# Performance work log

Hardware: AMD Instinct MI355X
Metric: run time of the kernel (lower is better)

The kernel has to match this reference:

```python
import jax, jax.numpy as jnp
import numpy as np
import math

B, L, LC = 2, 2048, 2048
D_MODEL, D_CROSS, D_HEAD = 1024, 1024, 64
N_HEADS = D_MODEL // D_HEAD
D6 = D_HEAD // 6  # freq bands per spatial axis (k-diffusion AxialRoPE, 3 axes)
EPS = 1e-6


def rope_freqs():
    n = N_HEADS * D6
    f = jnp.exp(jnp.linspace(math.log(math.pi), math.log(10.0 * math.pi), n + 1)[:-1])
    return f.reshape(D6, N_HEADS).T  # [nh, d6]


def rope_theta(pos):
    # pos: [b, l, 3] -> theta: [b, nh, l, 3*d6]
    f = rope_freqs()
    th = jnp.concatenate([pos[..., None, a:a + 1] * f for a in range(3)], axis=-1)  # [b,l,nh,3*d6]
    return jnp.moveaxis(th, -2, -3)


def apply_rotary(x, theta):
    d = theta.shape[-1]
    x1, x2, x3 = x[..., :d], x[..., d:2 * d], x[..., 2 * d:]
    c, s = jnp.cos(theta), jnp.sin(theta)
    return jnp.concatenate([x1 * c - x2 * s, x2 * c + x1 * s, x3], axis=-1)


def rms_norm(x, scale, eps=EPS):
    ms = jnp.mean(x * x, axis=-1, keepdims=True)
    return x * (scale * jax.lax.rsqrt(ms + eps))


def cosine_scale(q, k, scale, eps=EPS):
    s = jnp.sqrt(scale)[:, None, None]  # [nh,1,1]
    qn = q * (s * jax.lax.rsqrt(jnp.sum(q * q, axis=-1, keepdims=True) + eps))
    kn = k * (s * jax.lax.rsqrt(jnp.sum(k * k, axis=-1, keepdims=True) + eps))
    return qn, kn


def setup_inputs():
    key = jax.random.key(0)
    ks = jax.random.split(key, 8)
    return {
        "x": jax.random.normal(ks[0], (B, L, D_MODEL), jnp.float32),
        "pos": jax.random.uniform(ks[1], (B, L, 3), jnp.float32),
        "x_cross": jax.random.normal(ks[2], (B, LC, D_CROSS), jnp.float32),
        "pos_cross": jax.random.uniform(ks[3], (B, LC, 3), jnp.float32),
        "norm_scale": jnp.ones((D_MODEL,), jnp.float32),
        "norm_cross_scale": jnp.ones((D_CROSS,), jnp.float32),
        "q_w": jax.random.normal(ks[4], (D_MODEL, D_MODEL), jnp.float32) * 0.02,
        "kv_w": jax.random.normal(ks[5], (2 * D_MODEL, D_CROSS), jnp.float32) * 0.02,
        "head_scale": jnp.full((N_HEADS,), 10.0, jnp.float32),
        "out_w": jax.random.normal(ks[6], (D_MODEL, D_MODEL), jnp.float32) * 0.02,
    }


def reference(x, pos, x_cross, pos_cross, norm_scale, norm_cross_scale, q_w, kv_w, head_scale, out_w):
    skip = x
    xn = rms_norm(x, norm_scale)
    xc = rms_norm(x_cross, norm_cross_scale)
    q = xn @ q_w.T                       # [b,l,d]
    kv = xc @ kv_w.T                     # [b,lc,2d]
    b, l, _ = q.shape
    lc = kv.shape[1]
    q = q.reshape(b, l, N_HEADS, D_HEAD).transpose(0, 2, 1, 3)          # [b,nh,l,e]
    kv = kv.reshape(b, lc, 2, N_HEADS, D_HEAD)                          # (t nh e) factorization
    k = kv[:, :, 0].transpose(0, 2, 1, 3)
    v = kv[:, :, 1].transpose(0, 2, 1, 3)
    q, k = cosine_scale(q, k, head_scale)
    q = apply_rotary(q, rope_theta(pos))
    k = apply_rotary(k, rope_theta(pos_cross))
    attn = jax.nn.softmax(jnp.einsum('bhqe,bhke->bhqk', q, k), axis=-1)  # scale=1.0 (cosine-sim pre-scaled)
    o = jnp.einsum('bhqk,bhke->bhqe', attn, v)
    o = o.transpose(0, 2, 1, 3).reshape(b, l, D_MODEL)
    return o @ out_w.T + skip
```

## Files before the change

kernel.cpp:

```cpp
#include <hip/hip_runtime.h>

typedef __bf16 bf16_t;
typedef __bf16 bf16x4 __attribute__((ext_vector_type(4)));
typedef __bf16 bf16x8 __attribute__((ext_vector_type(8)));
typedef float f32x4 __attribute__((ext_vector_type(4)));
typedef short s16x4 __attribute__((ext_vector_type(4)));

#define B_DIM 2
#define L_DIM 2048
#define LC_DIM 2048
#define DM 1024
#define NH 16
#define DH 64
#define MB (1u << 20)
#define LOG2E 1.44269504088896f

__device__ __forceinline__ bool probe_is_f32(const unsigned* probe) {
  return probe[0] == 0x3F800000u;
}

__device__ __forceinline__ void async16(const bf16_t* g, bf16_t* l) {
  __builtin_amdgcn_global_load_lds((const __attribute__((address_space(1))) void*)g,
                                   (__attribute__((address_space(3))) void*)l, 16, 0, 0);
}

#if __has_builtin(__builtin_amdgcn_mfma_f32_16x16x16bf16_1k)
#define HAVE_K16 1
__device__ __forceinline__ f32x4 mfma16(bf16x4 a, bf16x4 b, f32x4 c) {
  union { bf16x4 h; s16x4 s; } ua, ub;
  ua.h = a; ub.h = b;
  return __builtin_amdgcn_mfma_f32_16x16x16bf16_1k(ua.s, ub.s, c, 0, 0, 0);
}
#else
#define HAVE_K16 0
#endif

__device__ __forceinline__ void conv_b(const void* src, bf16_t* dst, int i, bool f32) {
  bf16x4 w;
  if (f32) {
    f32x4 v = *(const f32x4*)((const float*)src + i);
    w[0] = (bf16_t)v[0]; w[1] = (bf16_t)v[1]; w[2] = (bf16_t)v[2]; w[3] = (bf16_t)v[3];
  } else {
    w = *(const bf16x4*)((const bf16_t*)src + i);
  }
  *(bf16x4*)(dst + i) = w;
}
__device__ __forceinline__ void conv_f(const void* src, float* dst, int i, int n, bool f32) {
  if (i >= n) return;
  f32x4 v;
  if (f32) {
    v = *(const f32x4*)((const float*)src + i);
  } else {
    bf16x4 w = *(const bf16x4*)((const bf16_t*)src + i);
    v[0] = (float)w[0]; v[1] = (float)w[1]; v[2] = (float)w[2]; v[3] = (float)w[3];
  }
  *(f32x4*)(dst + i) = v;
}

__global__ __launch_bounds__(256) void conv_all_k(
    const void* qw, const void* kvw, const void* ow, const void* pos,
    const void* posc, const void* ns, const void* ncs, const void* hs,
    bf16_t* cqw, bf16_t* ckvw, bf16_t* cow, float* fpos, float* fposc,
    float* fns, float* fncs, float* fhs, const unsigned* probe) {
  const bool f32 = probe_is_f32(probe);
  const int blk = blockIdx.x;
  const int e4 = threadIdx.x * 4;
  if (blk < 1024)       conv_b(qw,  cqw,  blk * 1024 + e4, f32);
  else if (blk < 3072)  conv_b(kvw, ckvw, (blk - 1024) * 1024 + e4, f32);
  else if (blk < 4096)  conv_b(ow,  cow,  (blk - 3072) * 1024 + e4, f32);
  else if (blk < 4108)  conv_f(pos,  fpos,  (blk - 4096) * 1024 + e4, 12288, f32);
  else if (blk < 4120)  conv_f(posc, fposc, (blk - 4108) * 1024 + e4, 12288, f32);
  else if (blk == 4120) conv_f(ns,  fns,  e4, 1024, f32);
  else if (blk == 4121) conv_f(ncs, fncs, e4, 1024, f32);
  else                  conv_f(hs,  fhs,  e4, 16, f32);
}

__global__ __launch_bounds__(256) void norm_both_k(const void* __restrict__ srcA,
                                                   const void* __restrict__ srcB,
                                                   const float* __restrict__ scA,
                                                   const float* __restrict__ scB,
                                                   bf16_t* __restrict__ outA,
                                                   bf16_t* __restrict__ outB,
                                                   const unsigned* __restrict__ probe) {
  const bool isB = blockIdx.x >= B_DIM * L_DIM;
  const int row = isB ? blockIdx.x - B_DIM * L_DIM : blockIdx.x;
  const void* src = isB ? srcB : srcA;
  const float* scale = isB ? scB : scA;
  bf16_t* out = isB ? outB : outA;
  const int tid = threadIdx.x;
  float f0, f1, f2, f3;
  if (probe_is_f32(probe)) {
    f32x4 v = *((const f32x4*)((const float*)src + (size_t)row * DM) + tid);
    f0 = v[0]; f1 = v[1]; f2 = v[2]; f3 = v[3];
  } else {
    bf16x4 v = *((const bf16x4*)((const bf16_t*)src + (size_t)row * DM) + tid);
    f0 = (float)v[0]; f1 = (float)v[1]; f2 = (float)v[2]; f3 = (float)v[3];
  }
  float ss = f0 * f0 + f1 * f1 + f2 * f2 + f3 * f3;
#pragma unroll
  for (int m = 1; m < 64; m <<= 1) ss += __shfl_xor(ss, m, 64);
  __shared__ float red[4];
  const int wave = tid >> 6, lane = tid & 63;
  if (lane == 0) red[wave] = ss;
  __syncthreads();
  float ms = (red[0] + red[1] + red[2] + red[3]) * (1.0f / DM);
  float r = rsqrtf(ms + 1e-6f);
  f32x4 sc = *(const f32x4*)(scale + tid * 4);
  bf16x4 w;
  w[0] = (bf16_t)(f0 * r * sc[0]);
  w[1] = (bf16_t)(f1 * r * sc[1]);
  w[2] = (bf16_t)(f2 * r * sc[2]);
  w[3] = (bf16_t)(f3 * r * sc[3]);
  *(bf16x4*)(out + (size_t)row * DM + tid * 4) = w;
}

__global__ __launch_bounds__(256) void gemm_qkv_k(const bf16_t* __restrict__ xn,
                                                  const bf16_t* __restrict__ xcn,
                                                  const bf16_t* __restrict__ qw,
                                                  const bf16_t* __restrict__ kvw,
                                                  bf16_t* __restrict__ qb,
                                                  bf16_t* __restrict__ kvK,
                                                  bf16_t* __restrict__ Vp) {
  __shared__ bf16_t Asm[128 * 32];
  __shared__ bf16_t Wsm[128 * 32];
  const int tid = threadIdx.x;
  const int wave = tid >> 6, lane = tid & 63;
  const int quad = lane >> 4, tc = lane & 15;
  const int wr = wave >> 1, wc = wave & 1;
  const bool isq = blockIdx.y < 8;
  const bf16_t* A = isq ? xn : xcn;
  const bf16_t* W = isq ? qw : kvw;
  const int n0 = (isq ? blockIdx.y : (blockIdx.y - 8)) * 128;
  const int m0 = blockIdx.x * 128;
  const int K = 1024;

  const int srow = wave * 16 + (lane >> 2);
  const int scol = (lane & 3) * 8;
  const bf16_t* ag = A + (size_t)(m0 + srow) * K + scol;
  const bf16_t* wg = W + (size_t)(n0 + srow) * K + scol;
  bf16_t* al0 = &Asm[(wave * 16) * 32];
  bf16_t* al1 = &Asm[(64 + wave * 16) * 32];
  bf16_t* wl0 = &Wsm[(wave * 16) * 32];
  bf16_t* wl1 = &Wsm[(64 + wave * 16) * 32];

  f32x4 acc[4][4] = {};

  for (int k0 = 0; k0 < K; k0 += 32) {
    async16(ag + k0, al0);
    async16(ag + k0 + (size_t)64 * K, al1);
    async16(wg + k0, wl0);
    async16(wg + k0 + (size_t)64 * K, wl1);
    __syncthreads();
    bf16x8 af[4], wf[4];
#pragma unroll
    for (int i = 0; i < 4; ++i)
      af[i] = *(const bf16x8*)&Asm[(wr * 64 + i * 16 + tc) * 32 + quad * 8];
#pragma unroll
    for (int j = 0; j < 4; ++j)
      wf[j] = *(const bf16x8*)&Wsm[(wc * 64 + j * 16 + tc) * 32 + quad * 8];
#pragma unroll
    for (int i = 0; i < 4; ++i)
#pragma unroll
      for (int j = 0; j < 4; ++j)
        acc[i][j] = __builtin_amdgcn_mfma_f32_16x16x32_bf16(af[i], wf[j], acc[i][j], 0, 0, 0);
    __syncthreads();
  }

  if (isq || n0 < DM) {
    bf16_t* C = isq ? qb : kvK;
#pragma unroll
    for (int i = 0; i < 4; ++i) {
      const size_t row = (size_t)m0 + wr * 64 + i * 16 + quad * 4;
#pragma unroll
      for (int j = 0; j < 4; ++j) {
        const int col = n0 + wc * 64 + j * 16 + tc;
#pragma unroll
        for (int r = 0; r < 4; ++r)
          C[(row + r) * DM + col] = (bf16_t)acc[i][j][r];
      }
    }
  } else {
#pragma unroll
    for (int i = 0; i < 4; ++i) {
      const int row = m0 + wr * 64 + i * 16 + quad * 4;
      const int b = row >> 11, kc = row & (LC_DIM - 1);
#pragma unroll
      for (int j = 0; j < 4; ++j) {
        const int hd = n0 - DM + wc * 64 + j * 16 + tc;
        const int h = hd >> 6, d = hd & 63;
        bf16x4 pk;
        pk[0] = (bf16_t)acc[i][j][0];
        pk[1] = (bf16_t)acc[i][j][1];
        pk[2] = (bf16_t)acc[i][j][2];
        pk[3] = (bf16_t)acc[i][j][3];
        *(bf16x4*)(Vp + (((size_t)(b * NH + h) * (LC_DIM / 4) + (kc >> 2)) * DH + d) * 4) = pk;
      }
    }
  }
}

__global__ __launch_bounds__(256) void prep_k(bf16_t* __restrict__ q,
                                              const bf16_t* __restrict__ kvK,
                                              bf16_t* __restrict__ Kp,
                                              const float* __restrict__ pos,
                                              const float* __restrict__ pos_cross,
                                              const float* __restrict__ head_scale) {
  const int gw = (blockIdx.x * blockDim.x + threadIdx.x) >> 6;
  const int lane = threadIdx.x & 63;
  const int per = B_DIM * L_DIM * NH;
  const bool is_k = gw >= per;
  const int id = is_k ? gw - per : gw;
  const int h = id & 15;
  const int row = id >> 4;
  const bf16_t* src = (is_k ? kvK : q) + (size_t)row * DM + h * DH;
  const float* pp = (is_k ? pos_cross : pos) + (size_t)row * 3;

  float val = (float)src[lane];
  float ss = val * val;
#pragma unroll
  for (int m = 1; m < 64; m <<= 1) ss += __shfl_xor(ss, m, 64);
  float sc = sqrtf(head_scale[h]) * rsqrtf(ss + 1e-6f);
  if (!is_k) sc *= LOG2E;
  float vn = val * sc;

  const int j = lane;
  const int tj = j < 30 ? j : (j < 60 ? j - 30 : 0);
  const int a = tj >= 20 ? 2 : (tj >= 10 ? 1 : 0);
  const int jj = tj - a * 10;
  float p = pp[a];
  float freq = 3.14159265358979f * expf((float)(jj * 16 + h) * 0.014391156831f);
  float th = p * freq;
  float cth = cosf(th), sth = sinf(th);
  const int partner = j < 30 ? j + 30 : (j < 60 ? j - 30 : j);
  float vp = __shfl(vn, partner, 64);
  float outv;
  if (j < 30)       outv = vn * cth - vp * sth;
  else if (j < 60)  outv = vn * cth + vp * sth;
  else              outv = vn;

  if (is_k) {
    const int b = row >> 11, l = row & (LC_DIM - 1);
    Kp[(((size_t)b * NH + h) * LC_DIM + l) * DH + lane] = (bf16_t)outv;
  } else {
    q[(size_t)row * DM + h * DH + lane] = (bf16_t)outv;
  }
}

__global__ __launch_bounds__(64) void flash5_k(const bf16_t* __restrict__ q,
                                               const bf16_t* __restrict__ Kp,
                                               const bf16_t* __restrict__ Vp,
                                               bf16_t* __restrict__ Op,
                                               float* __restrict__ lp) {
  const int lane = threadIdx.x;
  const int quad = lane >> 4, tc = lane & 15;
  const int bh = blockIdx.y, b = bh >> 4;
  const int z = blockIdx.z;
  const int q0 = blockIdx.x * 64;

  bf16x8 qf[4][2];
#pragma unroll
  for (int jj = 0; jj < 4; ++jj)
#pragma unroll
    for (int hf = 0; hf < 2; ++hf)
      qf[jj][hf] = *(const bf16x8*)(q + (size_t)(b * L_DIM + q0 + jj * 16 + tc) * DM +
                                    (bh & 15) * DH + hf * 32 + quad * 8);

  f32x4 accO[4][4] = {};
  const bf16_t* kg = Kp + (size_t)bh * LC_DIM * DH;
  const bf16_t* vp = Vp + (size_t)bh * (LC_DIM / 4) * DH * 4;

#if HAVE_K16
  f32x4 accL[4] = {};
  bf16x4 ones;
  ones[0] = (bf16_t)1.0f; ones[1] = (bf16_t)1.0f;
  ones[2] = (bf16_t)1.0f; ones[3] = (bf16_t)1.0f;
#else
  __shared__ bf16_t Psm[64 * 64];
  float lsum[4] = {0.f, 0.f, 0.f, 0.f};
  const int sw = tc & 7;
#endif

#pragma unroll 1
  for (int kc0 = z * 1024; kc0 < z * 1024 + 1024; kc0 += 64) {
    bf16x8 kfr[4][2];
#pragma unroll
    for (int mt = 0; mt < 4; ++mt)
#pragma unroll
      for (int hf = 0; hf < 2; ++hf)
        kfr[mt][hf] = *(const bf16x8*)(kg + (size_t)(kc0 + mt * 16 + tc) * DH +
                                       hf * 32 + quad * 8);

#if HAVE_K16
    bf16x4 vf[4][4];
#pragma unroll
    for (int mt = 0; mt < 4; ++mt)
#pragma unroll
      for (int dt = 0; dt < 4; ++dt)
        vf[mt][dt] = *(const bf16x4*)(vp + ((size_t)((kc0 >> 2) + mt * 4 + quad) * DH +
                                            dt * 16 + tc) * 4);

#pragma unroll
    for (int jj = 0; jj < 4; ++jj) {
      f32x4 s[4];
#pragma unroll
      for (int mt = 0; mt < 4; ++mt) {
        f32x4 zf = {0.f, 0.f, 0.f, 0.f};
        zf = __builtin_amdgcn_mfma_f32_16x16x32_bf16(kfr[mt][0], qf[jj][0], zf, 0, 0, 0);
        zf = __builtin_amdgcn_mfma_f32_16x16x32_bf16(kfr[mt][1], qf[jj][1], zf, 0, 0, 0);
        s[mt] = zf;
      }
      bf16x4 p[4];
#pragma unroll
      for (int mt = 0; mt < 4; ++mt) {
        p[mt][0] = (bf16_t)__builtin_amdgcn_exp2f(s[mt][0]);
        p[mt][1] = (bf16_t)__builtin_amdgcn_exp2f(s[mt][1]);
        p[mt][2] = (bf16_t)__builtin_amdgcn_exp2f(s[mt][2]);
        p[mt][3] = (bf16_t)__builtin_amdgcn_exp2f(s[mt][3]);
      }
#pragma unroll
      for (int mt = 0; mt < 4; ++mt) {
        accL[jj] = mfma16(p[mt], ones, accL[jj]);
#pragma unroll
        for (int dt = 0; dt < 4; ++dt)
          accO[jj][dt] = mfma16(p[mt], vf[mt][dt], accO[jj][dt]);
      }
    }
#else
#pragma unroll
    for (int jj = 0; jj < 4; ++jj) {
      f32x4 s[4];
#pragma unroll
      for (int mt = 0; mt < 4; ++mt) {
        f32x4 zf = {0.f, 0.f, 0.f, 0.f};
        zf = __builtin_amdgcn_mfma_f32_16x16x32_bf16(kfr[mt][0], qf[jj][0], zf, 0, 0, 0);
        zf = __builtin_amdgcn_mfma_f32_16x16x32_bf16(kfr[mt][1], qf[jj][1], zf, 0, 0, 0);
        s[mt] = zf;
      }
#pragma unroll
      for (int mt = 0; mt < 4; ++mt) {
        float p0 = __builtin_amdgcn_exp2f(s[mt][0]);
        float p1 = __builtin_amdgcn_exp2f(s[mt][1]);
        float p2 = __builtin_amdgcn_exp2f(s[mt][2]);
        float p3 = __builtin_amdgcn_exp2f(s[mt][3]);
        lsum[jj] += (p0 + p1) + (p2 + p3);
        bf16x4 pk;
        pk[0] = (bf16_t)p0; pk[1] = (bf16_t)p1; pk[2] = (bf16_t)p2; pk[3] = (bf16_t)p3;
        const int phys = (mt * 2 + (quad >> 1)) ^ sw;
        *(bf16x4*)&Psm[(jj * 16 + tc) * 64 + phys * 8 + (quad & 1) * 4] = pk;
      }
    }
#pragma unroll
    for (int kb = 0; kb < 2; ++kb) {
      bf16x8 vfull[4];
#pragma unroll
      for (int dt = 0; dt < 4; ++dt) {
        const size_t k4 = (size_t)((kc0 + kb * 32) >> 2) + quad * 2;
        bf16x4 lo = *(const bf16x4*)(vp + (k4 * DH + dt * 16 + tc) * 4);
        bf16x4 hi = *(const bf16x4*)(vp + ((k4 + 1) * DH + dt * 16 + tc) * 4);
#pragma unroll
        for (int e = 0; e < 4; ++e) { vfull[dt][e] = lo[e]; vfull[dt][4 + e] = hi[e]; }
      }
#pragma unroll
      for (int jp = 0; jp < 4; ++jp) {
        bf16x8 pf = *(const bf16x8*)&Psm[(jp * 16 + tc) * 64 + ((kb * 4 + quad) ^ sw) * 8];
#pragma unroll
        for (int dt = 0; dt < 4; ++dt)
          accO[jp][dt] = __builtin_amdgcn_mfma_f32_16x16x32_bf16(pf, vfull[dt], accO[jp][dt], 0, 0, 0);
      }
    }
#endif
  }

  bf16_t* Ob = Op + (size_t)(z * 32 + bh) * L_DIM * DH;
  float* lb = lp + (size_t)(z * 32 + bh) * L_DIM;
#if HAVE_K16
#pragma unroll
  for (int jj = 0; jj < 4; ++jj) {
    if (tc == 0) {
#pragma unroll
      for (int r = 0; r < 4; ++r) lb[q0 + jj * 16 + quad * 4 + r] = accL[jj][r];
    }
#pragma unroll
    for (int r = 0; r < 4; ++r) {
      const size_t qg = q0 + jj * 16 + quad * 4 + r;
#pragma unroll
      for (int dt = 0; dt < 4; ++dt)
        Ob[qg * DH + dt * 16 + tc] = (bf16_t)accO[jj][dt][r];
    }
  }
#else
#pragma unroll
  for (int jj = 0; jj < 4; ++jj) {
    lsum[jj] += __shfl_xor(lsum[jj], 16, 64);
    lsum[jj] += __shfl_xor(lsum[jj], 32, 64);
  }
#pragma unroll
  for (int jj = 0; jj < 4; ++jj) {
    if (quad == 0) lb[q0 + jj * 16 + tc] = lsum[jj];
#pragma unroll
    for (int r = 0; r < 4; ++r) {
      const size_t qg = q0 + jj * 16 + quad * 4 + r;
#pragma unroll
      for (int dt = 0; dt < 4; ++dt)
        Ob[qg * DH + dt * 16 + tc] = (bf16_t)accO[jj][dt][r];
    }
  }
#endif
}

__global__ __launch_bounds__(256) void combine_k(const bf16_t* __restrict__ Op,
                                                 const float* __restrict__ lp,
                                                 bf16_t* __restrict__ ob) {
  const size_t t = (size_t)blockIdx.x * 256 + threadIdx.x;
  const int bh = (int)(t >> 15);
  const int rem = (int)(t & 32767);
  const int l = rem >> 4, d4 = (rem & 15) * 4;
  const size_t base = ((size_t)bh * L_DIM + l) * DH + d4;
  const size_t zoff = (size_t)32 * L_DIM * DH;
  bf16x4 a0 = *(const bf16x4*)(Op + base);
  bf16x4 a1 = *(const bf16x4*)(Op + zoff + base);
  const float linv = 1.f / (lp[(size_t)bh * L_DIM + l] + lp[(size_t)32 * L_DIM + bh * L_DIM + l]);
  bf16x4 w;
#pragma unroll
  for (int e = 0; e < 4; ++e) w[e] = (bf16_t)(((float)a0[e] + (float)a1[e]) * linv);
  const int b = bh >> 4, h = bh & 15;
  *(bf16x4*)(ob + ((size_t)(b * L_DIM + l)) * DM + h * DH + d4) = w;
}

__global__ __launch_bounds__(256) void gemm_out_k(const bf16_t* __restrict__ A,
                                                  const bf16_t* __restrict__ W,
                                                  const void* __restrict__ skip_raw,
                                                  void* __restrict__ out,
                                                  const unsigned* __restrict__ probe) {
  __shared__ bf16_t Asm[64 * 32];
  __shared__ bf16_t Wsm[128 * 32];
  const int tid = threadIdx.x;
  const int wave = tid >> 6, lane = tid & 63;
  const int quad = lane >> 4, tc = lane & 15;
  const int wr = wave >> 1, wc = wave & 1;
  const int m0 = blockIdx.x * 64, n0 = blockIdx.y * 128;
  const int K = 1024, N = 1024;

  const int srow = wave * 16 + (lane >> 2);
  const int scol = (lane & 3) * 8;
  const bf16_t* ag = A + (size_t)(m0 + srow) * K + scol;
  const bf16_t* wg = W + (size_t)(n0 + srow) * K + scol;
  bf16_t* al = &Asm[(wave * 16) * 32];
  bf16_t* wl0 = &Wsm[(wave * 16) * 32];
  bf16_t* wl1 = &Wsm[(64 + wave * 16) * 32];

  f32x4 acc[2][4] = {};

  for (int k0 = 0; k0 < K; k0 += 32) {
    async16(ag + k0, al);
    async16(wg + k0, wl0);
    async16(wg + k0 + (size_t)64 * K, wl1);
    __syncthreads();
    bf16x8 af[2], wf[4];
#pragma unroll
    for (int i = 0; i < 2; ++i)
      af[i] = *(const bf16x8*)&Asm[(wr * 32 + i * 16 + tc) * 32 + quad * 8];
#pragma unroll
    for (int j = 0; j < 4; ++j)
      wf[j] = *(const bf16x8*)&Wsm[(wc * 64 + j * 16 + tc) * 32 + quad * 8];
#pragma unroll
    for (int i = 0; i < 2; ++i)
#pragma unroll
      for (int j = 0; j < 4; ++j)
        acc[i][j] = __builtin_amdgcn_mfma_f32_16x16x32_bf16(af[i], wf[j], acc[i][j], 0, 0, 0);
    __syncthreads();
  }

  const bool f32o = probe_is_f32(probe);
#pragma unroll
  for (int i = 0; i < 2; ++i) {
    const size_t row = (size_t)m0 + wr * 32 + i * 16 + quad * 4;
#pragma unroll
    for (int j = 0; j < 4; ++j) {
      const int col = n0 + wc * 64 + j * 16 + tc;
#pragma unroll
      for (int r = 0; r < 4; ++r) {
        const size_t idx = (row + r) * (size_t)N + col;
        float v = acc[i][j][r];
        if (f32o) {
          v += ((const float*)skip_raw)[idx];
          ((float*)out)[idx] = v;
        } else {
          v += (float)((const bf16_t*)skip_raw)[idx];
          ((bf16_t*)out)[idx] = (bf16_t)v;
        }
      }
    }
  }
}

extern "C" void kernel_launch(void* const* d_in, const int* in_sizes, int n_in,
                              void* d_out, int out_size, void* d_ws, size_t ws_size,
                              hipStream_t stream) {
  const unsigned* probe = (const unsigned*)d_in[4];
  char* ws = (char*)d_ws;

  bf16_t* cow  = (bf16_t*)(ws + 0 * MB);
  bf16_t* cqw  = (bf16_t*)(ws + 2 * MB);
  bf16_t* ckvw = (bf16_t*)(ws + 4 * MB);
  bf16_t* xn   = (bf16_t*)(ws + 8 * MB);
  bf16_t* xcn  = (bf16_t*)(ws + 16 * MB);
  bf16_t* Op   = (bf16_t*)(ws + 8 * MB);
  bf16_t* kvK  = (bf16_t*)(ws + 24 * MB);
  bf16_t* qb   = (bf16_t*)(ws + 32 * MB);
  bf16_t* Vp   = (bf16_t*)(ws + 40 * MB);
  bf16_t* Kp   = (bf16_t*)(ws + 48 * MB);
  bf16_t* ob   = (bf16_t*)(ws + 56 * MB);
  float* lp    = (float*)(ws + 64 * MB);
  float* fpos  = (float*)(ws + 65 * MB);
  float* fposc = (float*)(ws + 65 * MB + 64 * 1024);
  float* fns   = (float*)(ws + 65 * MB + 128 * 1024);
  float* fncs  = (float*)(ws + 65 * MB + 144 * 1024);
  float* fhs   = (float*)(ws + 65 * MB + 160 * 1024);

  conv_all_k<<<4123, 256, 0, stream>>>(d_in[6], d_in[7], d_in[9], d_in[1], d_in[3],
                                       d_in[4], d_in[5], d_in[8],
                                       cqw, ckvw, cow, fpos, fposc, fns, fncs, fhs, probe);
  norm_both_k<<<2 * B_DIM * L_DIM, 256, 0, stream>>>(d_in[0], d_in[2], fns, fncs,
                                                     xn, xcn, probe);
  gemm_qkv_k<<<dim3(32, 24), 256, 0, stream>>>(xn, xcn, cqw, ckvw, qb, kvK, Vp);
  prep_k<<<(2 * B_DIM * L_DIM * NH) / 4, 256, 0, stream>>>(qb, kvK, Kp, fpos, fposc, fhs);
  flash5_k<<<dim3(L_DIM / 64, B_DIM * NH, 2), 64, 0, stream>>>(qb, Kp, Vp, Op, lp);
  combine_k<<<4096, 256, 0, stream>>>(Op, lp, ob);
  gemm_out_k<<<dim3(64, 8), 256, 0, stream>>>(ob, cow, d_in[0], d_out, probe);
}
```

Baseline: 269.3 us.

## Fuse norm into conversion kernel and halve flash query tile to 32 rows

```diff
diff --git a/kernel.cpp b/kernel.cpp
--- a/kernel.cpp
+++ b/kernel.cpp
@@ -57,14 +57,51 @@
   *(f32x4*)(dst + i) = v;
 }
 
-__global__ __launch_bounds__(256) void conv_all_k(
-    const void* qw, const void* kvw, const void* ow, const void* pos,
-    const void* posc, const void* ns, const void* ncs, const void* hs,
-    bf16_t* cqw, bf16_t* ckvw, bf16_t* cow, float* fpos, float* fposc,
-    float* fns, float* fncs, float* fhs, const unsigned* probe) {
+__global__ __launch_bounds__(256) void front_k(
+    const void* x, const void* xc, const void* qw, const void* kvw, const void* ow,
+    const void* pos, const void* posc, const void* ns, const void* ncs, const void* hs,
+    bf16_t* xn, bf16_t* xcn, bf16_t* cqw, bf16_t* ckvw, bf16_t* cow,
+    float* fpos, float* fposc, float* fns, float* fncs, float* fhs,
+    const unsigned* probe) {
   const bool f32 = probe_is_f32(probe);
-  const int blk = blockIdx.x;
-  const int e4 = threadIdx.x * 4;
+  const int tid = threadIdx.x;
+  if (blockIdx.x < 2 * B_DIM * L_DIM) {
+    const bool isB = blockIdx.x >= B_DIM * L_DIM;
+    const int row = isB ? blockIdx.x - B_DIM * L_DIM : blockIdx.x;
+    const void* src = isB ? xc : x;
+    const void* scr = isB ? ncs : ns;
+    bf16_t* out = isB ? xcn : xn;
+    float f0, f1, f2, f3, s0, s1, s2, s3;
+    if (f32) {
+      f32x4 v = *((const f32x4*)((const float*)src + (size_t)row * DM) + tid);
+      f0 = v[0]; f1 = v[1]; f2 = v[2]; f3 = v[3];
+      f32x4 sv = *((const f32x4*)scr + tid);
+      s0 = sv[0]; s1 = sv[1]; s2 = sv[2]; s3 = sv[3];
+    } else {
+      bf16x4 v = *((const bf16x4*)((const bf16_t*)src + (size_t)row * DM) + tid);
+      f0 = (float)v[0]; f1 = (float)v[1]; f2 = (float)v[2]; f3 = (float)v[3];
+      bf16x4 sv = *((const bf16x4*)scr + tid);
+      s0 = (float)sv[0]; s1 = (float)sv[1]; s2 = (float)sv[2]; s3 = (float)sv[3];
+    }
+    float ss = f0 * f0 + f1 * f1 + f2 * f2 + f3 * f3;
+#pragma unroll
+    for (int m = 1; m < 64; m <<= 1) ss += __shfl_xor(ss, m, 64);
+    __shared__ float red[4];
+    const int wave = tid >> 6, lane = tid & 63;
+    if (lane == 0) red[wave] = ss;
+    __syncthreads();
+    float ms = (red[0] + red[1] + red[2] + red[3]) * (1.0f / DM);
+    float r = rsqrtf(ms + 1e-6f);
+    bf16x4 w;
+    w[0] = (bf16_t)(f0 * r * s0);
+    w[1] = (bf16_t)(f1 * r * s1);
+    w[2] = (bf16_t)(f2 * r * s2);
+    w[3] = (bf16_t)(f3 * r * s3);
+    *(bf16x4*)(out + (size_t)row * DM + tid * 4) = w;
+    return;
+  }
+  const int blk = blockIdx.x - 2 * B_DIM * L_DIM;
+  const int e4 = tid * 4;
   if (blk < 1024)       conv_b(qw,  cqw,  blk * 1024 + e4, f32);
   else if (blk < 3072)  conv_b(kvw, ckvw, (blk - 1024) * 1024 + e4, f32);
   else if (blk < 4096)  conv_b(ow,  cow,  (blk - 3072) * 1024 + e4, f32);
@@ -73,45 +110,6 @@
   else if (blk == 4120) conv_f(ns,  fns,  e4, 1024, f32);
   else if (blk == 4121) conv_f(ncs, fncs, e4, 1024, f32);
   else                  conv_f(hs,  fhs,  e4, 16, f32);
-}
-
-__global__ __launch_bounds__(256) void norm_both_k(const void* __restrict__ srcA,
-                                                   const void* __restrict__ srcB,
-                                                   const float* __restrict__ scA,
-                                                   const float* __restrict__ scB,
-                                                   bf16_t* __restrict__ outA,
-                                                   bf16_t* __restrict__ outB,
-                                                   const unsigned* __restrict__ probe) {
-  const bool isB = blockIdx.x >= B_DIM * L_DIM;
-  const int row = isB ? blockIdx.x - B_DIM * L_DIM : blockIdx.x;
-  const void* src = isB ? srcB : srcA;
-  const float* scale = isB ? scB : scA;
-  bf16_t* out = isB ? outB : outA;
-  const int tid = threadIdx.x;
-  float f0, f1, f2, f3;
-  if (probe_is_f32(probe)) {
-    f32x4 v = *((const f32x4*)((const float*)src + (size_t)row * DM) + tid);
-    f0 = v[0]; f1 = v[1]; f2 = v[2]; f3 = v[3];
-  } else {
-    bf16x4 v = *((const bf16x4*)((const bf16_t*)src + (size_t)row * DM) + tid);
-    f0 = (float)v[0]; f1 = (float)v[1]; f2 = (float)v[2]; f3 = (float)v[3];
-  }
-  float ss = f0 * f0 + f1 * f1 + f2 * f2 + f3 * f3;
-#pragma unroll
-  for (int m = 1; m < 64; m <<= 1) ss += __shfl_xor(ss, m, 64);
-  __shared__ float red[4];
-  const int wave = tid >> 6, lane = tid & 63;
-  if (lane == 0) red[wave] = ss;
-  __syncthreads();
-  float ms = (red[0] + red[1] + red[2] + red[3]) * (1.0f / DM);
-  float r = rsqrtf(ms + 1e-6f);
-  f32x4 sc = *(const f32x4*)(scale + tid * 4);
-  bf16x4 w;
-  w[0] = (bf16_t)(f0 * r * sc[0]);
-  w[1] = (bf16_t)(f1 * r * sc[1]);
-  w[2] = (bf16_t)(f2 * r * sc[2]);
-  w[3] = (bf16_t)(f3 * r * sc[3]);
-  *(bf16x4*)(out + (size_t)row * DM + tid * 4) = w;
 }
 
 __global__ __launch_bounds__(256) void gemm_qkv_k(const bf16_t* __restrict__ xn,
@@ -246,37 +244,37 @@
   }
 }
 
-__global__ __launch_bounds__(64) void flash5_k(const bf16_t* __restrict__ q,
-                                               const bf16_t* __restrict__ Kp,
-                                               const bf16_t* __restrict__ Vp,
-                                               bf16_t* __restrict__ Op,
-                                               float* __restrict__ lp) {
+__global__ __launch_bounds__(64, 4) void flash6_k(const bf16_t* __restrict__ q,
+                                                  const bf16_t* __restrict__ Kp,
+                                                  const bf16_t* __restrict__ Vp,
+                                                  bf16_t* __restrict__ Op,
+                                                  float* __restrict__ lp) {
   const int lane = threadIdx.x;
   const int quad = lane >> 4, tc = lane & 15;
   const int bh = blockIdx.y, b = bh >> 4;
   const int z = blockIdx.z;
-  const int q0 = blockIdx.x * 64;
-
-  bf16x8 qf[4][2];
-#pragma unroll
-  for (int jj = 0; jj < 4; ++jj)
+  const int q0 = blockIdx.x * 32;
+
+  bf16x8 qf[2][2];
+#pragma unroll
+  for (int jj = 0; jj < 2; ++jj)
 #pragma unroll
     for (int hf = 0; hf < 2; ++hf)
       qf[jj][hf] = *(const bf16x8*)(q + (size_t)(b * L_DIM + q0 + jj * 16 + tc) * DM +
                                     (bh & 15) * DH + hf * 32 + quad * 8);
 
-  f32x4 accO[4][4] = {};
+  f32x4 accO[2][4] = {};
   const bf16_t* kg = Kp + (size_t)bh * LC_DIM * DH;
   const bf16_t* vp = Vp + (size_t)bh * (LC_DIM / 4) * DH * 4;
 
 #if HAVE_K16
-  f32x4 accL[4] = {};
+  f32x4 accL[2] = {};
   bf16x4 ones;
   ones[0] = (bf16_t)1.0f; ones[1] = (bf16_t)1.0f;
   ones[2] = (bf16_t)1.0f; ones[3] = (bf16_t)1.0f;
 #else
-  __shared__ bf16_t Psm[64 * 64];
-  float lsum[4] = {0.f, 0.f, 0.f, 0.f};
+  __shared__ bf16_t Psm[32 * 64];
+  float lsum[2] = {0.f, 0.f};
   const int sw = tc & 7;
 #endif
 
@@ -300,7 +298,7 @@
                                             dt * 16 + tc) * 4);
 
 #pragma unroll
-    for (int jj = 0; jj < 4; ++jj) {
+    for (int jj = 0; jj < 2; ++jj) {
       f32x4 s[4];
 #pragma unroll
       for (int mt = 0; mt < 4; ++mt) {
@@ -327,7 +325,7 @@
     }
 #else
 #pragma unroll
-    for (int jj = 0; jj < 4; ++jj) {
+    for (int jj = 0; jj < 2; ++jj) {
       f32x4 s[4];
 #pragma unroll
       for (int mt = 0; mt < 4; ++mt) {
@@ -361,7 +359,7 @@
         for (int e = 0; e < 4; ++e) { vfull[dt][e] = lo[e]; vfull[dt][4 + e] = hi[e]; }
       }
 #pragma unroll
-      for (int jp = 0; jp < 4; ++jp) {
+      for (int jp = 0; jp < 2; ++jp) {
         bf16x8 pf = *(const bf16x8*)&Psm[(jp * 16 + tc) * 64 + ((kb * 4 + quad) ^ sw) * 8];
 #pragma unroll
         for (int dt = 0; dt < 4; ++dt)
@@ -375,7 +373,7 @@
   float* lb = lp + (size_t)(z * 32 + bh) * L_DIM;
 #if HAVE_K16
 #pragma unroll
-  for (int jj = 0; jj < 4; ++jj) {
+  for (int jj = 0; jj < 2; ++jj) {
     if (tc == 0) {
 #pragma unroll
       for (int r = 0; r < 4; ++r) lb[q0 + jj * 16 + quad * 4 + r] = accL[jj][r];
@@ -390,12 +388,12 @@
   }
 #else
 #pragma unroll
-  for (int jj = 0; jj < 4; ++jj) {
+  for (int jj = 0; jj < 2; ++jj) {
     lsum[jj] += __shfl_xor(lsum[jj], 16, 64);
     lsum[jj] += __shfl_xor(lsum[jj], 32, 64);
   }
 #pragma unroll
-  for (int jj = 0; jj < 4; ++jj) {
+  for (int jj = 0; jj < 2; ++jj) {
     if (quad == 0) lb[q0 + jj * 16 + tc] = lsum[jj];
 #pragma unroll
     for (int r = 0; r < 4; ++r) {
@@ -518,14 +516,12 @@
   float* fncs  = (float*)(ws + 65 * MB + 144 * 1024);
   float* fhs   = (float*)(ws + 65 * MB + 160 * 1024);
 
-  conv_all_k<<<4123, 256, 0, stream>>>(d_in[6], d_in[7], d_in[9], d_in[1], d_in[3],
-                                       d_in[4], d_in[5], d_in[8],
-                                       cqw, ckvw, cow, fpos, fposc, fns, fncs, fhs, probe);
-  norm_both_k<<<2 * B_DIM * L_DIM, 256, 0, stream>>>(d_in[0], d_in[2], fns, fncs,
-                                                     xn, xcn, probe);
+  front_k<<<2 * B_DIM * L_DIM + 4123, 256, 0, stream>>>(
+      d_in[0], d_in[2], d_in[6], d_in[7], d_in[9], d_in[1], d_in[3], d_in[4],
+      d_in[5], d_in[8], xn, xcn, cqw, ckvw, cow, fpos, fposc, fns, fncs, fhs, probe);
   gemm_qkv_k<<<dim3(32, 24), 256, 0, stream>>>(xn, xcn, cqw, ckvw, qb, kvK, Vp);
   prep_k<<<(2 * B_DIM * L_DIM * NH) / 4, 256, 0, stream>>>(qb, kvK, Kp, fpos, fposc, fhs);
-  flash5_k<<<dim3(L_DIM / 64, B_DIM * NH, 2), 64, 0, stream>>>(qb, Kp, Vp, Op, lp);
+  flash6_k<<<dim3(L_DIM / 32, B_DIM * NH, 2), 64, 0, stream>>>(qb, Kp, Vp, Op, lp);
   combine_k<<<4096, 256, 0, stream>>>(Op, lp, ob);
   gemm_out_k<<<dim3(64, 8), 256, 0, stream>>>(ob, cow, d_in[0], d_out, probe);
 }
```

Result: slower. 293.1 us (+8.8%).
